# Optimization experiments

Measured on AMD Instinct MI355X. Metric: run time of the kernel, lower is better.

Reference implementation:

```python
import jax, jax.numpy as jnp
import numpy as np

H = W = 224
WS = 7          # window size
SS = 3          # shift size
NH = 12         # num heads
N = WS * WS     # tokens per window (49)


def _attn_mask():
    # shift-window attention mask, computed from static ints (numpy)
    img = np.zeros((H, W), np.float32)
    cnt = 0
    for h0, h1 in [(0, H - WS), (H - WS, H - SS), (H - SS, H)]:
        for w0, w1 in [(0, W - WS), (W - WS, W - SS), (W - SS, W)]:
            img[h0:h1, w0:w1] = cnt
            cnt += 1
    mw = img.reshape(H // WS, WS, W // WS, WS).transpose(0, 2, 1, 3).reshape(-1, N)
    diff = mw[:, None, :] - mw[:, :, None]          # (nW, N, N)
    m = np.where(diff != 0, -100.0, 0.0).astype(np.float32)
    return m[:, None, :, :]                         # (nW, 1, N, N)


def _rel_pos_index():
    coords = np.stack(np.meshgrid(np.arange(WS), np.arange(WS), indexing='ij'))
    cf = coords.reshape(2, -1)
    rc = (cf[:, :, None] - cf[:, None, :]).transpose(1, 2, 0)  # (N, N, 2)
    rc[..., 0] += WS - 1
    rc[..., 1] += WS - 1
    rc[..., 0] *= 2 * WS - 1
    return rc.sum(-1).reshape(-1)                    # (N*N,)


_MASK = _attn_mask()
_RPI = _rel_pos_index()


def _ln(x, w, b, eps=1e-5):
    mu = jnp.mean(x, -1, keepdims=True)
    var = jnp.mean((x - mu) ** 2, -1, keepdims=True)
    return (x - mu) / jnp.sqrt(var + eps) * w + b


def setup_inputs() -> dict:
    key = jax.random.key(0)
    ks = jax.random.split(key, 12)
    C, CM = 384, 1536
    s = 0.02
    return {
        'x': jax.random.normal(ks[0], (1, H * W, C), jnp.float32),
        'rpb_table': jax.random.normal(ks[1], (169, NH), jnp.float32) * s,
        'qkv_w': jax.random.normal(ks[2], (3 * C, C), jnp.float32) * s,
        'qkv_b': jax.random.normal(ks[3], (3 * C,), jnp.float32) * s,
        'proj_w': jax.random.normal(ks[4], (C, C), jnp.float32) * s,
        'proj_b': jax.random.normal(ks[5], (C,), jnp.float32) * s,
        'fc1_w': jax.random.normal(ks[6], (CM, C), jnp.float32) * s,
        'fc1_b': jax.random.normal(ks[7], (CM,), jnp.float32) * s,
        'fc2_w': jax.random.normal(ks[8], (C, CM), jnp.float32) * s,
        'fc2_b': jax.random.normal(ks[9], (C,), jnp.float32) * s,
        'norm1_w': jnp.ones((C,), jnp.float32),
        'norm1_b': jnp.zeros((C,), jnp.float32),
        'norm2_w': jnp.ones((C,), jnp.float32),
        'norm2_b': jnp.zeros((C,), jnp.float32),
    }


def reference(x, rpb_table, qkv_w, qkv_b, proj_w, proj_b, fc1_w, fc1_b,
              fc2_w, fc2_b, norm1_w, norm1_b, norm2_w, norm2_b):
    B, L, C = x.shape
    hd = C // NH
    scale = hd ** -0.5
    mask = jnp.asarray(_MASK)                        # (nW, 1, N, N)
    rpi = jnp.asarray(_RPI)

    shortcut = x
    h = _ln(x, norm1_w, norm1_b).reshape(B, H, W, C)
    h = jnp.roll(h, (-SS, -SS), axis=(1, 2))
    # window partition -> (B*nW, N, C)
    win = h.reshape(B, H // WS, WS, W // WS, WS, C).transpose(0, 1, 3, 2, 4, 5)
    win = win.reshape(-1, N, C)

    qkv = (win @ qkv_w.T + qkv_b).reshape(-1, N, 3, NH, hd).transpose(2, 0, 3, 1, 4)
    q, k, v = qkv[0] * scale, qkv[1], qkv[2]         # (nW, NH, N, hd)
    attn = jnp.einsum('whnd,whmd->whnm', q, k)
    bias = rpb_table[rpi].reshape(N, N, NH).transpose(2, 0, 1)[None]  # (1, NH, N, N)
    attn = jax.nn.softmax(attn + bias + mask, axis=-1)
    out = jnp.einsum('whnm,whmd->whnd', attn, v).transpose(0, 2, 1, 3).reshape(-1, N, C)
    out = out @ proj_w.T + proj_b

    # window reverse + unshift
    h = out.reshape(B, H // WS, W // WS, WS, WS, C).transpose(0, 1, 3, 2, 4, 5)
    h = h.reshape(B, H, W, C)
    h = jnp.roll(h, (SS, SS), axis=(1, 2)).reshape(B, L, C)

    x = shortcut + h
    y = _ln(x, norm2_w, norm2_b)
    y = jax.nn.gelu(y @ fc1_w.T + fc1_b, approximate=False)  # torch nn.GELU = erf
    y = y @ fc2_w.T + fc2_b
    return x + y
```

## Files before the change

kernel.cpp:

```cpp
#include <hip/hip_runtime.h>
#include <cstdint>
#include <cstddef>

#define AS1 __attribute__((address_space(1)))
#define AS3 __attribute__((address_space(3)))

typedef __attribute__((ext_vector_type(8))) short bf16x8;
typedef __attribute__((ext_vector_type(4))) short short4v;
typedef __attribute__((ext_vector_type(8))) unsigned short u16x8;
typedef __attribute__((ext_vector_type(4))) float f32x4;
typedef __attribute__((ext_vector_type(4))) unsigned short u16x4;

__device__ __forceinline__ float b2f(uint16_t u){ return __uint_as_float(((uint32_t)u) << 16); }
__device__ __forceinline__ uint16_t f2b(float f){
    uint32_t u = __float_as_uint(f);
    return (uint16_t)((u + 0x7fffu + ((u >> 16) & 1u)) >> 16);
}

__device__ __forceinline__ int pixof(int r){
    int w  = r / 49, t = r - w * 49;
    int wh = w >> 5, ww = w & 31;
    int th = t / 7,  tw = t - th * 7;
    int hp = wh * 7 + th + 3; if (hp >= 224) hp -= 224;
    int wp = ww * 7 + tw + 3; if (wp >= 224) wp -= 224;
    return hp * 224 + wp;
}

__global__ void f2b4_kernel(const float* __restrict__ a0, const float* __restrict__ a1,
                            const float* __restrict__ a2, const float* __restrict__ a3,
                            uint16_t* __restrict__ o0, uint16_t* __restrict__ o1,
                            uint16_t* __restrict__ o2, uint16_t* __restrict__ o3){
    int b = blockIdx.x;
    const float* src; uint16_t* dst; int base;
    if (b < 1728)      { src = a0; dst = o0; base = b; }
    else if (b < 2304) { src = a1; dst = o1; base = b - 1728; }
    else if (b < 4608) { src = a2; dst = o2; base = b - 2304; }
    else               { src = a3; dst = o3; base = b - 4608; }
    int i = base * 256 + threadIdx.x;
    dst[i] = f2b(src[i]);
}

template<int PERM>
__global__ __launch_bounds__(256) void ln_kernel(const float* __restrict__ in,
        const float* __restrict__ g, const float* __restrict__ b, uint16_t* __restrict__ out){
    int wave = threadIdx.x >> 6, lane = threadIdx.x & 63;
    int r = blockIdx.x * 4 + wave;
    int p = PERM ? pixof(r) : r;
    const float* row = in + (size_t)p * 384;
    float a[6];
    #pragma unroll
    for (int i = 0; i < 6; ++i) a[i] = row[lane * 6 + i];
    float s = 0.f, q = 0.f;
    #pragma unroll
    for (int i = 0; i < 6; ++i){ s += a[i]; q += a[i] * a[i]; }
    #pragma unroll
    for (int o = 32; o; o >>= 1){ s += __shfl_xor(s, o); q += __shfl_xor(q, o); }
    float mu   = s * (1.f / 384.f);
    float var  = q * (1.f / 384.f) - mu * mu;
    float rstd = rsqrtf(var + 1e-5f);
    uint16_t* orow = out + (size_t)r * 384;
    #pragma unroll
    for (int i = 0; i < 6; ++i){
        int c = lane * 6 + i;
        orow[c] = f2b((a[i] - mu) * rstd * g[c] + b[c]);
    }
}

template<int EPI>
__global__ __launch_bounds__(256, 2) void gemm_bt(
        const uint16_t* __restrict__ A, const uint16_t* __restrict__ B,
        const float* __restrict__ bias, void* __restrict__ outp,
        const float* __restrict__ xres, int N, int K, int row0)
{
    __shared__ alignas(16) uint16_t lA[128 * 64];
    __shared__ alignas(16) uint16_t lB[128 * 64];
    int tid  = threadIdx.x;
    int lane = tid & 63, wave = tid >> 6;

    int nwg = gridDim.x, bid = blockIdx.x;
    int q8 = nwg >> 3, r8 = nwg & 7;
    int xcd = bid & 7, idx = bid >> 3;
    int wg = (xcd < r8 ? xcd * (q8 + 1) : r8 * (q8 + 1) + (xcd - r8) * q8) + idx;

    int nt = N >> 7;
    int bm = wg / nt, bn = wg - bm * nt;
    int wr = wave >> 1, wc = wave & 1;
    int fr = lane & 15, kc = lane >> 4;

    int srow = wave * 32 + (lane >> 3);
    int cs   = (lane & 7) ^ ((lane >> 3) & 7);
    const uint16_t* gA = A + (size_t)(bm * 128 + srow) * K + cs * 8;
    const uint16_t* gB = B + (size_t)(bn * 128 + srow) * K + cs * 8;

    int aoff[4], boff[4];
    #pragma unroll
    for (int m = 0; m < 4; ++m){
        int row = wr * 64 + m * 16 + fr;
        aoff[m] = row * 128 + ((kc * 16) ^ ((row & 7) << 4));
        int rowB = wc * 64 + m * 16 + fr;
        boff[m] = rowB * 128 + ((kc * 16) ^ ((rowB & 7) << 4));
    }

    f32x4 acc[4][4] = {};
    const int NT = K >> 6;
    for (int t = 0; t < NT; ++t){
        int k0 = t << 6;
        #pragma unroll
        for (int it = 0; it < 4; ++it){
            __builtin_amdgcn_global_load_lds((const AS1 void*)(gA + k0 + (size_t)it * 8 * K),
                (AS3 void*)((AS3 char*)lA + wave * 4096 + it * 1024), 16, 0, 0);
            __builtin_amdgcn_global_load_lds((const AS1 void*)(gB + k0 + (size_t)it * 8 * K),
                (AS3 void*)((AS3 char*)lB + wave * 4096 + it * 1024), 16, 0, 0);
        }
        __syncthreads();

        #pragma unroll
        for (int ks = 0; ks < 2; ++ks){
            bf16x8 af[4], bv[4];
            #pragma unroll
            for (int m = 0; m < 4; ++m)
                af[m] = *(const bf16x8*)((const char*)lA + (aoff[m] ^ (ks << 6)));
            #pragma unroll
            for (int n = 0; n < 4; ++n)
                bv[n] = *(const bf16x8*)((const char*)lB + (boff[n] ^ (ks << 6)));
            #pragma unroll
            for (int m = 0; m < 4; ++m)
                #pragma unroll
                for (int n = 0; n < 4; ++n)
                    acc[m][n] = __builtin_amdgcn_mfma_f32_16x16x32_bf16(af[m], bv[n], acc[m][n], 0, 0, 0);
        }
        __syncthreads();
    }

    int colb = bn * 128 + wc * 64 + fr;
    int rowb = bm * 128 + wr * 64 + ((lane >> 4) << 2);
    float bvv[4];
    #pragma unroll
    for (int n = 0; n < 4; ++n) bvv[n] = bias[colb + n * 16];

    if constexpr (EPI == 0 || EPI == 1 || EPI == 5){
        uint16_t* out = (uint16_t*)outp;
        #pragma unroll
        for (int m = 0; m < 4; ++m)
            #pragma unroll
            for (int rg = 0; rg < 4; ++rg){
                size_t rr = (size_t)(rowb + m * 16 + rg) * N;
                #pragma unroll
                for (int n = 0; n < 4; ++n){
                    int col = colb + n * 16;
                    float v = acc[m][n][rg] + bvv[n];
                    if constexpr (EPI == 1) v = 0.5f * v * (1.f + erff(v * 0.7071067811865475f));
                    if constexpr (EPI == 5){ if (col < 384) v *= 0.1767766952966369f; }
                    out[rr + col] = f2b(v);
                }
            }
    } else if constexpr (EPI == 2){
        float* out = (float*)outp;
        #pragma unroll
        for (int m = 0; m < 4; ++m)
            #pragma unroll
            for (int rg = 0; rg < 4; ++rg){
                int r = row0 + rowb + m * 16 + rg;
                size_t pb = (size_t)pixof(r) * 384;
                #pragma unroll
                for (int n = 0; n < 4; ++n){
                    int c = colb + n * 16;
                    out[pb + c] = xres[pb + c] + acc[m][n][rg] + bvv[n];
                }
            }
    } else {
        float* out = (float*)outp;
        #pragma unroll
        for (int m = 0; m < 4; ++m)
            #pragma unroll
            for (int rg = 0; rg < 4; ++rg){
                size_t rb2 = (size_t)(rowb + m * 16 + rg) * 384;
                #pragma unroll
                for (int n = 0; n < 4; ++n){
                    int c = colb + n * 16;
                    out[rb2 + c] = out[rb2 + c] + acc[m][n][rg] + bvv[n];
                }
            }
    }
}

__global__ __launch_bounds__(256) void attn_mfma(const uint16_t* __restrict__ qkv,
        const float* __restrict__ rpb, uint16_t* __restrict__ out)
{
    __shared__ float bl[4][208];
    __shared__ uint16_t vtl[4][32][68];
    int wv = threadIdx.x >> 6, lane = threadIdx.x & 63;
    int p = blockIdx.x * 4 + wv;
    int w = p / 12, h = p - w * 12;
    for (int i = lane; i < 169; i += 64) bl[wv][i] = rpb[i * 12 + h];

    const uint16_t* base = qkv + (size_t)(w * 49) * 1152 + h * 32;

    #pragma unroll
    for (int it = 0; it < 4; ++it){
        int u = it * 64 + lane;
        int t = u >> 2, dq = u & 3;
        if (t < 49){
            u16x8 v8 = *(const u16x8*)(base + (size_t)t * 1152 + 768 + dq * 8);
            #pragma unroll
            for (int j = 0; j < 8; ++j) vtl[wv][dq * 8 + j][t] = v8[j];
        } else {
            #pragma unroll
            for (int j = 0; j < 8; ++j) vtl[wv][dq * 8 + j][t] = 0;
        }
    }

    int c = lane & 15, g = lane >> 4;

    bf16x8 qf[4], kf[4];
    #pragma unroll
    for (int nt = 0; nt < 4; ++nt) qf[nt] = *(const bf16x8*)(base + (size_t)(16 * nt + c) * 1152 + g * 8);
    #pragma unroll
    for (int mt = 0; mt < 4; ++mt) kf[mt] = *(const bf16x8*)(base + (size_t)(16 * mt + c) * 1152 + 384 + g * 8);

    f32x4 zero = {0.f, 0.f, 0.f, 0.f};
    f32x4 sv[4][4];
    #pragma unroll
    for (int mt = 0; mt < 4; ++mt)
        #pragma unroll
        for (int nt = 0; nt < 4; ++nt)
            sv[mt][nt] = __builtin_amdgcn_mfma_f32_16x16x32_bf16(kf[mt], qf[nt], zero, 0, 0, 0);

    int wh = w >> 5, ww = w & 31;
    bool edge = (wh == 31) || (ww == 31);
    int ihq[4], iwq[4], regi[4];
    #pragma unroll
    for (int nt = 0; nt < 4; ++nt){
        int q = 16 * nt + c;
        int ih = (q * 37) >> 8; int iw = q - 7 * ih;
        ihq[nt] = ih; iwq[nt] = iw;
        int hi = wh * 7 + ih, wi = ww * 7 + iw;
        regi[nt] = (hi < 217 ? 0 : (hi < 221 ? 1 : 2)) * 3 + (wi < 217 ? 0 : (wi < 221 ? 1 : 2));
    }
    #pragma unroll
    for (int mt = 0; mt < 4; ++mt){
        #pragma unroll
        for (int r = 0; r < 4; ++r){
            int kt = 16 * mt + 4 * g + r;
            int jh = (kt * 37) >> 8; int jw = kt - 7 * jh;
            int hj = wh * 7 + jh, wj = ww * 7 + jw;
            int regj = (hj < 217 ? 0 : (hj < 221 ? 1 : 2)) * 3 + (wj < 217 ? 0 : (wj < 221 ? 1 : 2));
            #pragma unroll
            for (int nt = 0; nt < 4; ++nt){
                float b = bl[wv][(ihq[nt] - jh + 6) * 13 + (iwq[nt] - jw + 6)];
                float add = b + ((edge && regj != regi[nt]) ? -100.f : 0.f);
                float val = sv[mt][nt][r] + add;
                sv[mt][nt][r] = (kt < 49) ? val : -1e9f;
            }
        }
    }

    float inv[4];
    #pragma unroll
    for (int nt = 0; nt < 4; ++nt){
        float mx = -1e30f;
        #pragma unroll
        for (int mt = 0; mt < 4; ++mt)
            #pragma unroll
            for (int r = 0; r < 4; ++r) mx = fmaxf(mx, sv[mt][nt][r]);
        mx = fmaxf(mx, __shfl_xor(mx, 16));
        mx = fmaxf(mx, __shfl_xor(mx, 32));
        float sum = 0.f;
        #pragma unroll
        for (int mt = 0; mt < 4; ++mt)
            #pragma unroll
            for (int r = 0; r < 4; ++r){
                float e = __expf(sv[mt][nt][r] - mx);
                sv[mt][nt][r] = e; sum += e;
            }
        sum += __shfl_xor(sum, 16);
        sum += __shfl_xor(sum, 32);
        inv[nt] = 1.f / sum;
    }

    unsigned pk[4][4][2];
    #pragma unroll
    for (int nt = 0; nt < 4; ++nt)
        #pragma unroll
        for (int mt = 0; mt < 4; ++mt)
            #pragma unroll
            for (int pr = 0; pr < 2; ++pr)
                pk[nt][mt][pr] = (unsigned)f2b(sv[mt][nt][2 * pr]) |
                                 ((unsigned)f2b(sv[mt][nt][2 * pr + 1]) << 16);

    int a0 = (c + 16 * (2 * (g & 1))) * 4;
    int a1 = a0 + 64;
    int sel = g >> 1;

    f32x4 acco[2][4] = {};
    #pragma unroll
    for (int ks = 0; ks < 2; ++ks){
        bf16x8 va[2];
        #pragma unroll
        for (int mt = 0; mt < 2; ++mt){
            short4v lo = *(const short4v*)&vtl[wv][mt * 16 + c][ks * 32 + g * 8];
            short4v hi = *(const short4v*)&vtl[wv][mt * 16 + c][ks * 32 + g * 8 + 4];
            bf16x8 t;
            t[0] = lo[0]; t[1] = lo[1]; t[2] = lo[2]; t[3] = lo[3];
            t[4] = hi[0]; t[5] = hi[1]; t[6] = hi[2]; t[7] = hi[3];
            va[mt] = t;
        }
        #pragma unroll
        for (int nt = 0; nt < 4; ++nt){
            union { unsigned u[4]; bf16x8 v; } pb;
            #pragma unroll
            for (int t = 0; t < 4; ++t){
                int addr = (t >> 1) ? a1 : a0;
                unsigned lo = (unsigned)__builtin_amdgcn_ds_bpermute(addr, (int)pk[nt][2 * ks][t & 1]);
                unsigned hi = (unsigned)__builtin_amdgcn_ds_bpermute(addr, (int)pk[nt][2 * ks + 1][t & 1]);
                pb.u[t] = sel ? hi : lo;
            }
            #pragma unroll
            for (int mt = 0; mt < 2; ++mt)
                acco[mt][nt] = __builtin_amdgcn_mfma_f32_16x16x32_bf16(va[mt], pb.v, acco[mt][nt], 0, 0, 0);
        }
    }

    #pragma unroll
    for (int mt = 0; mt < 2; ++mt)
        #pragma unroll
        for (int nt = 0; nt < 4; ++nt){
            int q = 16 * nt + c;
            if (q < 49){
                u16x4 o;
                #pragma unroll
                for (int r = 0; r < 4; ++r) o[r] = f2b(acco[mt][nt][r] * inv[nt]);
                *(u16x4*)(out + (size_t)(w * 49 + q) * 384 + h * 32 + 16 * mt + 4 * g) = o;
            }
        }
}

extern "C" void kernel_launch(void* const* d_in, const int* in_sizes, int n_in,
                              void* d_out, int out_size, void* d_ws, size_t ws_size,
                              hipStream_t stream) {
    const float* x      = (const float*)d_in[0];
    const float* rpb    = (const float*)d_in[1];
    const float* qkv_w  = (const float*)d_in[2];
    const float* qkv_b  = (const float*)d_in[3];
    const float* proj_w = (const float*)d_in[4];
    const float* proj_b = (const float*)d_in[5];
    const float* fc1_w  = (const float*)d_in[6];
    const float* fc1_b  = (const float*)d_in[7];
    const float* fc2_w  = (const float*)d_in[8];
    const float* fc2_b  = (const float*)d_in[9];
    const float* n1w    = (const float*)d_in[10];
    const float* n1b    = (const float*)d_in[11];
    const float* n2w    = (const float*)d_in[12];
    const float* n2b    = (const float*)d_in[13];

    char* ws = (char*)d_ws;
    uint16_t* winA = (uint16_t*)ws;
    uint16_t* qkB  = (uint16_t*)(ws + 38535168);
    uint16_t* wbuf = (uint16_t*)(ws + 154140672);
    uint16_t* w_qkv  = wbuf;
    uint16_t* w_proj = wbuf + 442368;
    uint16_t* w_fc1  = w_proj + 147456;
    uint16_t* w_fc2  = w_fc1 + 589824;

    f2b4_kernel<<<6912, 256, 0, stream>>>(qkv_w, proj_w, fc1_w, fc2_w,
                                          w_qkv, w_proj, w_fc1, w_fc2);

    ln_kernel<1><<<12544, 256, 0, stream>>>(x, n1w, n1b, winA);

    gemm_bt<5><<<392 * 9, 256, 0, stream>>>(winA, w_qkv, qkv_b, qkB, nullptr, 1152, 384, 0);

    attn_mfma<<<3072, 256, 0, stream>>>(qkB, rpb, winA);

    gemm_bt<2><<<392 * 3, 256, 0, stream>>>(winA, w_proj, proj_b, d_out, x, 384, 384, 0);

    ln_kernel<0><<<12544, 256, 0, stream>>>((const float*)d_out, n2w, n2b, winA);

    for (int c2 = 0; c2 < 2; ++c2){
        size_t r0 = (size_t)c2 * 25088;
        gemm_bt<1><<<196 * 12, 256, 0, stream>>>(winA + r0 * 384, w_fc1, fc1_b, qkB, nullptr, 1536, 384, 0);
        gemm_bt<3><<<196 * 3, 256, 0, stream>>>(qkB, w_fc2, fc2_b, (float*)d_out + r0 * 384, nullptr, 384, 1536, 0);
    }
}
```

Measured before the change: 376.2 us.

## Precompute bias+mask tables per window type and feed them as MFMA accumulator init

A new small kernel builds a 64x64 table of relative-position bias plus shift mask for each of 4 window edge types and 12 heads. The attention kernel loads the table entries directly as the initial accumulator of the QK^T MFMA. This replaces the per-element index arithmetic, shared-memory bias gather and region comparisons, leaving only a fixed padding-column mask. It also keeps the V loads in registers until after QK^T before transposing them into shared memory, and raises wave priority around the MFMA blocks. The cost is an extra launch and about 786 KB of global table reads, which are mostly cache hits.

```diff
diff --git a/kernel.cpp b/kernel.cpp
--- a/kernel.cpp
+++ b/kernel.cpp
@@ -40,6 +40,25 @@
     dst[i] = f2b(src[i]);
 }
 
+__global__ void bm_init(const float* __restrict__ rpb, float* __restrict__ bm){
+    int th = blockIdx.x;
+    int type = th / 12, h = th - (th / 12) * 12;
+    int eh = type >> 1, ew = type & 1;
+    for (int idx = threadIdx.x; idx < 4096; idx += 256){
+        int q = idx >> 6, kt = idx & 63;
+        float v = 0.f;
+        if (q < 49 && kt < 49){
+            int ih = q / 7,  iw = q - 7 * (q / 7);
+            int jh = kt / 7, jw = kt - 7 * (kt / 7);
+            v = rpb[((ih - jh + 6) * 13 + (iw - jw + 6)) * 12 + h];
+            int ri = (eh ? (ih < 4 ? 1 : 2) : 0) * 3 + (ew ? (iw < 4 ? 1 : 2) : 0);
+            int rj = (eh ? (jh < 4 ? 1 : 2) : 0) * 3 + (ew ? (jw < 4 ? 1 : 2) : 0);
+            if (ri != rj) v -= 100.f;
+        }
+        bm[(size_t)th * 4096 + idx] = v;
+    }
+}
+
 template<int PERM>
 __global__ __launch_bounds__(256) void ln_kernel(const float* __restrict__ in,
         const float* __restrict__ g, const float* __restrict__ b, uint16_t* __restrict__ out){
@@ -185,32 +204,24 @@
 }
 
 __global__ __launch_bounds__(256) void attn_mfma(const uint16_t* __restrict__ qkv,
-        const float* __restrict__ rpb, uint16_t* __restrict__ out)
+        const float* __restrict__ bm, uint16_t* __restrict__ out)
 {
-    __shared__ float bl[4][208];
     __shared__ uint16_t vtl[4][32][68];
     int wv = threadIdx.x >> 6, lane = threadIdx.x & 63;
     int p = blockIdx.x * 4 + wv;
     int w = p / 12, h = p - w * 12;
-    for (int i = lane; i < 169; i += 64) bl[wv][i] = rpb[i * 12 + h];
-
+    int c = lane & 15, g = lane >> 4;
     const uint16_t* base = qkv + (size_t)(w * 49) * 1152 + h * 32;
 
+    u16x8 vreg[4];
     #pragma unroll
     for (int it = 0; it < 4; ++it){
         int u = it * 64 + lane;
         int t = u >> 2, dq = u & 3;
-        if (t < 49){
-            u16x8 v8 = *(const u16x8*)(base + (size_t)t * 1152 + 768 + dq * 8);
-            #pragma unroll
-            for (int j = 0; j < 8; ++j) vtl[wv][dq * 8 + j][t] = v8[j];
-        } else {
-            #pragma unroll
-            for (int j = 0; j < 8; ++j) vtl[wv][dq * 8 + j][t] = 0;
-        }
-    }
-
-    int c = lane & 15, g = lane >> 4;
+        u16x8 v8 = {0,0,0,0,0,0,0,0};
+        if (t < 49) v8 = *(const u16x8*)(base + (size_t)t * 1152 + 768 + dq * 8);
+        vreg[it] = v8;
+    }
 
     bf16x8 qf[4], kf[4];
     #pragma unroll
@@ -218,42 +229,33 @@
     #pragma unroll
     for (int mt = 0; mt < 4; ++mt) kf[mt] = *(const bf16x8*)(base + (size_t)(16 * mt + c) * 1152 + 384 + g * 8);
 
-    f32x4 zero = {0.f, 0.f, 0.f, 0.f};
+    int wh = w >> 5, ww = w & 31;
+    int type = ((wh == 31) << 1) | (ww == 31);
+    const float* bmp = bm + (size_t)(type * 12 + h) * 4096;
     f32x4 sv[4][4];
+    __builtin_amdgcn_s_setprio(1);
     #pragma unroll
     for (int mt = 0; mt < 4; ++mt)
         #pragma unroll
-        for (int nt = 0; nt < 4; ++nt)
-            sv[mt][nt] = __builtin_amdgcn_mfma_f32_16x16x32_bf16(kf[mt], qf[nt], zero, 0, 0, 0);
-
-    int wh = w >> 5, ww = w & 31;
-    bool edge = (wh == 31) || (ww == 31);
-    int ihq[4], iwq[4], regi[4];
-    #pragma unroll
-    for (int nt = 0; nt < 4; ++nt){
-        int q = 16 * nt + c;
-        int ih = (q * 37) >> 8; int iw = q - 7 * ih;
-        ihq[nt] = ih; iwq[nt] = iw;
-        int hi = wh * 7 + ih, wi = ww * 7 + iw;
-        regi[nt] = (hi < 217 ? 0 : (hi < 221 ? 1 : 2)) * 3 + (wi < 217 ? 0 : (wi < 221 ? 1 : 2));
-    }
-    #pragma unroll
-    for (int mt = 0; mt < 4; ++mt){
-        #pragma unroll
-        for (int r = 0; r < 4; ++r){
-            int kt = 16 * mt + 4 * g + r;
-            int jh = (kt * 37) >> 8; int jw = kt - 7 * jh;
-            int hj = wh * 7 + jh, wj = ww * 7 + jw;
-            int regj = (hj < 217 ? 0 : (hj < 221 ? 1 : 2)) * 3 + (wj < 217 ? 0 : (wj < 221 ? 1 : 2));
-            #pragma unroll
-            for (int nt = 0; nt < 4; ++nt){
-                float b = bl[wv][(ihq[nt] - jh + 6) * 13 + (iwq[nt] - jw + 6)];
-                float add = b + ((edge && regj != regi[nt]) ? -100.f : 0.f);
-                float val = sv[mt][nt][r] + add;
-                sv[mt][nt][r] = (kt < 49) ? val : -1e9f;
-            }
-        }
-    }
+        for (int nt = 0; nt < 4; ++nt){
+            f32x4 cb = *(const f32x4*)(bmp + (16 * nt + c) * 64 + 16 * mt + 4 * g);
+            sv[mt][nt] = __builtin_amdgcn_mfma_f32_16x16x32_bf16(kf[mt], qf[nt], cb, 0, 0, 0);
+        }
+    __builtin_amdgcn_s_setprio(0);
+
+    #pragma unroll
+    for (int it = 0; it < 4; ++it){
+        int u = it * 64 + lane;
+        int t = u >> 2, dq = u & 3;
+        #pragma unroll
+        for (int j = 0; j < 8; ++j) vtl[wv][dq * 8 + j][t] = vreg[it][j];
+    }
+
+    #pragma unroll
+    for (int nt = 0; nt < 4; ++nt)
+        #pragma unroll
+        for (int r = 0; r < 4; ++r)
+            if (4 * g + r >= 1) sv[3][nt][r] = -1e9f;
 
     float inv[4];
     #pragma unroll
@@ -305,20 +307,26 @@
             t[4] = hi[0]; t[5] = hi[1]; t[6] = hi[2]; t[7] = hi[3];
             va[mt] = t;
         }
+        bf16x8 pb[4];
         #pragma unroll
         for (int nt = 0; nt < 4; ++nt){
-            union { unsigned u[4]; bf16x8 v; } pb;
+            union { unsigned u[4]; bf16x8 v; } pbu;
             #pragma unroll
             for (int t = 0; t < 4; ++t){
                 int addr = (t >> 1) ? a1 : a0;
-                unsigned lo = (unsigned)__builtin_amdgcn_ds_bpermute(addr, (int)pk[nt][2 * ks][t & 1]);
-                unsigned hi = (unsigned)__builtin_amdgcn_ds_bpermute(addr, (int)pk[nt][2 * ks + 1][t & 1]);
-                pb.u[t] = sel ? hi : lo;
-            }
+                unsigned lo2 = (unsigned)__builtin_amdgcn_ds_bpermute(addr, (int)pk[nt][2 * ks][t & 1]);
+                unsigned hi2 = (unsigned)__builtin_amdgcn_ds_bpermute(addr, (int)pk[nt][2 * ks + 1][t & 1]);
+                pbu.u[t] = sel ? hi2 : lo2;
+            }
+            pb[nt] = pbu.v;
+        }
+        __builtin_amdgcn_s_setprio(1);
+        #pragma unroll
+        for (int nt = 0; nt < 4; ++nt)
             #pragma unroll
             for (int mt = 0; mt < 2; ++mt)
-                acco[mt][nt] = __builtin_amdgcn_mfma_f32_16x16x32_bf16(va[mt], pb.v, acco[mt][nt], 0, 0, 0);
-        }
+                acco[mt][nt] = __builtin_amdgcn_mfma_f32_16x16x32_bf16(va[mt], pb[nt], acco[mt][nt], 0, 0, 0);
+        __builtin_amdgcn_s_setprio(0);
     }
 
     #pragma unroll
@@ -361,15 +369,17 @@
     uint16_t* w_proj = wbuf + 442368;
     uint16_t* w_fc1  = w_proj + 147456;
     uint16_t* w_fc2  = w_fc1 + 589824;
+    float*    bmtab  = (float*)(ws + 157679616);
 
     f2b4_kernel<<<6912, 256, 0, stream>>>(qkv_w, proj_w, fc1_w, fc2_w,
                                           w_qkv, w_proj, w_fc1, w_fc2);
+    bm_init<<<48, 256, 0, stream>>>(rpb, bmtab);
 
     ln_kernel<1><<<12544, 256, 0, stream>>>(x, n1w, n1b, winA);
 
     gemm_bt<5><<<392 * 9, 256, 0, stream>>>(winA, w_qkv, qkv_b, qkB, nullptr, 1152, 384, 0);
 
-    attn_mfma<<<3072, 256, 0, stream>>>(qkB, rpb, winA);
+    attn_mfma<<<3072, 256, 0, stream>>>(qkB, bmtab, winA);
 
     gemm_bt<2><<<392 * 3, 256, 0, stream>>>(winA, w_proj, proj_b, d_out, x, 384, 384, 0);
 
```

Result: no change. 381.4 us (+1.4%).
